# Kernel tuning notes

Hardware: AMD Instinct MI355X
Metric: run time of the kernel (lower is better)

Reference implementation:

```python
import jax, jax.numpy as jnp
import numpy as np

NUM_USER = 20000
NUM_ITEM = 40000
N_NODES = NUM_USER + NUM_ITEM
DIM = 64
V_DIM = 2048
T_DIM = 768
N_EDGES = 1_000_000
K_USER = 40
K_ITEM = 10
N_LAYERS = 2


def setup_inputs() -> dict:
    key = jax.random.key(0)
    ks = iter(jax.random.split(key, 32))

    def xavier(shape):
        s = (2.0 / (shape[0] + shape[-1])) ** 0.5
        return jax.random.normal(next(ks), shape, jnp.float32) * s

    # bipartite user-item interactions, doubled (undirected), as in DRAGON.__init__
    u = jax.random.randint(next(ks), (N_EDGES,), 0, NUM_USER)
    it = jax.random.randint(next(ks), (N_EDGES,), NUM_USER, N_NODES)
    edge_index = jnp.stack([jnp.concatenate([u, it]), jnp.concatenate([it, u])])

    v_feat = jax.random.normal(next(ks), (NUM_ITEM, V_DIM), jnp.float32)
    t_feat = jax.random.normal(next(ks), (NUM_ITEM, T_DIM), jnp.float32)

    # KNN item-item adjacency (top-10 per row) with symmetric-normalized values,
    # mirroring get_knn_adj_mat/compute_normalized_laplacian
    rows = jnp.repeat(jnp.arange(NUM_ITEM), K_ITEM)
    cols = jax.random.randint(next(ks), (NUM_ITEM * K_ITEM,), 0, NUM_ITEM)
    mm_indices = jnp.stack([rows, cols])
    row_sum = jax.ops.segment_sum(jnp.ones(NUM_ITEM * K_ITEM, jnp.float32), rows,
                                  num_segments=NUM_ITEM) + 1e-7
    rinv = row_sum ** -0.5
    mm_values = rinv[rows] * rinv[cols]

    user_graph = jax.random.randint(next(ks), (NUM_USER, K_USER), 0, NUM_USER)
    user_weight_matrix = jax.nn.softmax(
        jax.random.normal(next(ks), (NUM_USER, K_USER), jnp.float32), axis=1)
    weight_u = jax.nn.softmax(
        jax.random.normal(next(ks), (NUM_USER, 2, 1), jnp.float32), axis=1)

    return {
        'edge_index': edge_index,
        'v_feat': v_feat, 't_feat': t_feat,
        'v_pref': xavier((NUM_USER, DIM)), 't_pref': xavier((NUM_USER, DIM)),
        'v_mlp1_w': xavier((V_DIM, 4 * DIM)), 'v_mlp1_b': jnp.zeros(4 * DIM, jnp.float32),
        'v_mlp2_w': xavier((4 * DIM, DIM)), 'v_mlp2_b': jnp.zeros(DIM, jnp.float32),
        't_mlp1_w': xavier((T_DIM, 4 * DIM)), 't_mlp1_b': jnp.zeros(4 * DIM, jnp.float32),
        't_mlp2_w': xavier((4 * DIM, DIM)), 't_mlp2_b': jnp.zeros(DIM, jnp.float32),
        'v_conv_w': xavier((DIM, DIM)), 'v_conv_b': jnp.zeros(DIM, jnp.float32),
        't_conv_w': xavier((DIM, DIM)), 't_conv_b': jnp.zeros(DIM, jnp.float32),
        'weight_u': weight_u,
        'user_graph': user_graph,
        'user_weight_matrix': user_weight_matrix,
        'mm_indices': mm_indices,
        'mm_values': mm_values,
    }


def _l2n(x):
    n = jnp.linalg.norm(x, axis=-1, keepdims=True)
    return x / jnp.maximum(n, 1e-12)


def reference(edge_index, v_feat, t_feat, v_pref, t_pref,
              v_mlp1_w, v_mlp1_b, v_mlp2_w, v_mlp2_b,
              t_mlp1_w, t_mlp1_b, t_mlp2_w, t_mlp2_b,
              v_conv_w, v_conv_b, t_conv_w, t_conv_b,
              weight_u, user_graph, user_weight_matrix,
              mm_indices, mm_values):
    seg = jax.ops.segment_sum
    # GCNConv normalization with self-loops (shared by both branches)
    sl = jnp.arange(N_NODES)
    src = jnp.concatenate([edge_index[0], sl])
    dst = jnp.concatenate([edge_index[1], sl])
    deg = seg(jnp.ones_like(dst, dtype=jnp.float32), dst, num_segments=N_NODES)
    dinv = deg ** -0.5
    norm = (dinv[src] * dinv[dst])[:, None]

    def conv(x, w, b):  # out[dst] += norm * (x @ w)[src], then bias
        return seg(norm * (x @ w)[src], dst, num_segments=N_NODES) + b

    def branch(feat, pref, w1, b1, w2, b2, cw, cb):
        temp = jax.nn.leaky_relu(feat @ w1 + b1) @ w2 + b2  # [I, D]
        x = _l2n(jnp.concatenate([pref, temp], axis=0))      # [N, D]
        h = conv(x, cw, cb)
        h1 = conv(h, cw, cb)
        return x + h + h1

    v_rep = branch(v_feat, v_pref, v_mlp1_w, v_mlp1_b, v_mlp2_w, v_mlp2_b, v_conv_w, v_conv_b)
    t_rep = branch(t_feat, t_pref, t_mlp1_w, t_mlp1_b, t_mlp2_w, t_mlp2_b, t_conv_w, t_conv_b)

    representation = jnp.concatenate([v_rep, t_rep], axis=1)  # [N, 2D]
    wu = weight_u[:, :, 0]  # [U, 2]
    user_rep = jnp.concatenate([wu[:, 0:1] * v_rep[:NUM_USER],
                                wu[:, 1:2] * t_rep[:NUM_USER]], axis=1)  # [U, 2D]
    item_rep = representation[NUM_USER:]  # [I, 2D]

    # User_Graph_sample: weighted sum over sampled user neighborhoods
    h_u = jnp.einsum('uk,ukd->ud', user_weight_matrix, user_rep[user_graph])
    user_rep = user_rep + h_u

    # n_layers of sparse Laplacian propagation over KNN item-item graph
    row, col = mm_indices[0], mm_indices[1]
    h_i = item_rep
    for _ in range(N_LAYERS):
        h_i = seg(mm_values[:, None] * h_i[col], row, num_segments=NUM_ITEM)
    item_rep = item_rep + h_i

    return jnp.concatenate([user_rep, item_rep], axis=0)  # [N, 2D]
```

## Files before the change

### kernel.cpp

```cpp
#include <hip/hip_runtime.h>

#define NUSER 20000
#define NITEM 40000
#define NNODE 60000
#define DIM   64
#define NE    1000000
#define KUSER 40
#define KITEM 10

typedef __attribute__((ext_vector_type(8))) short short8v;
typedef __attribute__((ext_vector_type(4))) float floatx4;

__device__ inline short bf16rne(float f) {
    unsigned u = __builtin_bit_cast(unsigned, f);
    unsigned r = (u + 0x7fffu + ((u >> 16) & 1u)) >> 16;
    return (short)r;
}
__device__ inline unsigned cvt_pk_bf16(float lo, float hi) {
    unsigned r;
    asm("v_cvt_pk_bf16_f32 %0, %1, %2" : "=v"(r) : "v"(lo), "v"(hi));
    return r;
}
__device__ inline float bflo(unsigned v) { return __builtin_bit_cast(float, v << 16); }
__device__ inline float bfhi(unsigned v) { return __builtin_bit_cast(float, v & 0xffff0000u); }

#define CNTB ((NE + 255) / 256)
#define TRB  2944
#define L2NB (NUSER * 2 / 4)
__global__ __launch_bounds__(256) void k_count_transpose_l2n(
        const int* __restrict__ uu, const int* __restrict__ it, int* __restrict__ cnt,
        const float* __restrict__ W1v, const float* __restrict__ W1t,
        const float* __restrict__ W2v, const float* __restrict__ W2t,
        short* __restrict__ Bv, short* __restrict__ Bt,
        short* __restrict__ B2v, short* __restrict__ B2t,
        const float* __restrict__ prefv, const float* __restrict__ preft,
        unsigned* __restrict__ xbf) {
    __shared__ float s[16][17];
    int bid = blockIdx.x;
    if (bid < CNTB) {
        int i = bid * 256 + threadIdx.x;
        if (i >= NE) return;
        atomicAdd(&cnt[uu[i]], 1);
        atomicAdd(&cnt[it[i]], 1);
        return;
    }
    bid -= CNTB;
    if (bid >= TRB) {
        int lb = bid - TRB;
        int lane = threadIdx.x & 63;
        int wg = lb * 4 + (threadIdx.x >> 6);
        int row = wg >> 1, br = wg & 1;
        if (row >= NUSER) return;
        const float* p = br ? preft : prefv;
        float v = p[(size_t)row * 64 + lane];
        float ss = v * v;
        #pragma unroll
        for (int off = 32; off >= 1; off >>= 1) ss += __shfl_xor(ss, off, 64);
        float xn = v / fmaxf(sqrtf(ss), 1e-12f);
        float pn = __shfl_xor(xn, 1, 64);
        if (!(lane & 1))
            xbf[(size_t)row * 64 + (br ? 32 : 0) + (lane >> 1)] = cvt_pk_bf16(xn, pn);
        return;
    }
    const float* B; short* D; int K, N, local;
    if (bid < 2048)      { B = W1v; D = Bv;  K = 2048; N = 256; local = bid; }
    else if (bid < 2816) { B = W1t; D = Bt;  K = 768;  N = 256; local = bid - 2048; }
    else if (bid < 2880) { B = W2v; D = B2v; K = 256;  N = 64;  local = bid - 2816; }
    else                 { B = W2t; D = B2t; K = 256;  N = 64;  local = bid - 2880; }
    int ktiles = K >> 4;
    int k0 = (local % ktiles) * 16, n0 = (local / ktiles) * 16;
    int t = threadIdx.x, tx = t & 15, ty = t >> 4;
    s[ty][tx] = B[(size_t)(k0 + ty) * N + n0 + tx];
    __syncthreads();
    int k = k0 + tx, n = n0 + ty;
    D[(size_t)(k >> 5) * (N * 32) + n * 32 + (k & 31)] = bf16rne(s[tx][ty]);
}

__global__ __launch_bounds__(256) void k_scanA(const int* __restrict__ v, int* __restrict__ excl,
                                               int* __restrict__ bsum, float* __restrict__ dinv, int n) {
    __shared__ int s[256];
    int t = threadIdx.x, i = blockIdx.x * 256 + t;
    int orig = (i < n) ? v[i] : 0;
    if (i < n) dinv[i] = 1.0f / sqrtf((float)(orig + 1));
    s[t] = orig; __syncthreads();
    #pragma unroll
    for (int off = 1; off < 256; off <<= 1) {
        int u = (t >= off) ? s[t - off] : 0;
        __syncthreads();
        s[t] += u;
        __syncthreads();
    }
    if (i < n) excl[i] = s[t] - orig;
    if (t == 255) bsum[blockIdx.x] = s[255];
}

__global__ __launch_bounds__(256) void k_scanB_prep(int* __restrict__ bsum, int nb,
                                                    const float* __restrict__ Wv, const float* __restrict__ Wt,
                                                    const float* __restrict__ bv, const float* __restrict__ bt,
                                                    short* __restrict__ Bcat, float* __restrict__ bw,
                                                    float* __restrict__ bb) {
    __shared__ float Wld[2][64][65];
    __shared__ float W2ld[2][64][65];
    int t = threadIdx.x;
    if (blockIdx.x == 0) {
        int* s = (int*)&Wld[0][0][0];
        int orig = (t < nb) ? bsum[t] : 0;
        s[t] = orig; __syncthreads();
        #pragma unroll
        for (int off = 1; off < 256; off <<= 1) {
            int u = (t >= off) ? s[t - off] : 0;
            __syncthreads();
            s[t] += u;
            __syncthreads();
        }
        if (t < nb) bsum[t] = s[t] - orig;
        return;
    }
    for (int id = t; id < 8192; id += 256) {
        int z = id >> 12, k = (id >> 6) & 63, n = id & 63;
        Wld[z][k][n] = (z ? Wt : Wv)[k * 64 + n];
    }
    __syncthreads();
    for (int id = t; id < 8192; id += 256) {
        int z = id >> 12, k = (id >> 6) & 63, n = id & 63;
        float a = 0.f;
        #pragma unroll 8
        for (int m = 0; m < 64; m++) a += Wld[z][k][m] * Wld[z][m][n];
        W2ld[z][k][n] = a;
    }
    __syncthreads();
    for (int id = t; id < 32768; id += 256) {
        int k = id >> 7, n = id & 127;
        int kb = k >> 6, kk = k & 63;
        float v = 0.f;
        if (kb == 0)      { if (n < 64)  v = Wld[0][kk][n]; }
        else if (kb == 1) { if (n >= 64) v = Wld[1][kk][n - 64]; }
        else if (kb == 2) { if (n < 64)  v = W2ld[0][kk][n]; }
        else              { if (n >= 64) v = W2ld[1][kk][n - 64]; }
        Bcat[(k >> 5) * 4096 + n * 32 + (k & 31)] = bf16rne(v);
    }
    if (t < 128) {
        int z = t >> 6, n = t & 63;
        const float* b = z ? bt : bv;
        float a = 0.f;
        #pragma unroll 8
        for (int k = 0; k < 64; k++) a += b[k] * Wld[z][k][n];
        bw[t] = a;
        bb[t] = 2.f * b[n];
    }
}

__global__ __launch_bounds__(256) void k_scanC(int* __restrict__ excl, const int* __restrict__ bsum,
                                               int* __restrict__ cursor, int n) {
    int i = blockIdx.x * 256 + threadIdx.x;
    if (i < n) {
        int v = excl[i] + bsum[blockIdx.x];
        excl[i] = v;
        cursor[i] = v;
    }
    if (i == 0) excl[n] = 2 * NE;
}

__global__ __launch_bounds__(256) void k_fill_pair(const int* __restrict__ uu, const int* __restrict__ it,
                                                   const float* __restrict__ dinv, int* __restrict__ cursor,
                                                   unsigned* __restrict__ csr_pkd) {
    int i = blockIdx.x * 256 + threadIdx.x;
    if (i >= NE) return;
    int u = uu[i], t = it[i];
    unsigned pku = ((unsigned)(unsigned short)bf16rne(dinv[u]) << 16) | (unsigned)u;
    unsigned pkt = ((unsigned)(unsigned short)bf16rne(dinv[t]) << 16) | (unsigned)t;
    int pos1 = atomicAdd(&cursor[t], 1);
    csr_pkd[pos1] = pku;
    int pos2 = atomicAdd(&cursor[u], 1);
    csr_pkd[pos2] = pkt;
}

#define AP   40
#define MIDP 264
#define MBLK 128
#define VBLKS ((NITEM + MBLK - 1) / MBLK)
__global__ __launch_bounds__(512, 4) void mlp_merged(const float* __restrict__ Av, const float* __restrict__ At,
                                                  const short* __restrict__ B1v, const short* __restrict__ B1t,
                                                  const float* __restrict__ b1v, const float* __restrict__ b1t,
                                                  const short* __restrict__ B2v, const short* __restrict__ B2t,
                                                  const float* __restrict__ b2v, const float* __restrict__ b2t,
                                                  unsigned* __restrict__ xbf) {
    __shared__ short smem[MBLK * MIDP];
    short* As = smem;
    short* Bs = smem + 2 * MBLK * AP;
    const bool isV = blockIdx.x < VBLKS;
    const float* A    = isV ? Av : At;
    const short* B1t_ = isV ? B1v : B1t;
    const float* b1   = isV ? b1v : b1t;
    const short* B2t_ = isV ? B2v : B2t;
    const float* b2   = isV ? b2v : b2t;
    const int K = isV ? 2048 : 768;
    const int boff = isV ? 0 : 32;
    const int rowBase = (isV ? blockIdx.x : blockIdx.x - VBLKS) * MBLK;

    const int tid = threadIdx.x;
    const int lane = tid & 63, wid = tid >> 6;
    const int wr = wid >> 2, wc = wid & 3;

    const int sar = tid >> 2, sac = (tid & 3) * 8;
    int aclamp = rowBase + sar; if (aclamp > NITEM - 1) aclamp = NITEM - 1;
    const float* aptr = A + (size_t)aclamp * K + sac;

    const int fk = (lane >> 4) * 8;
    const int faoff = (wr * 64 + (lane & 15)) * AP + fk;
    const int fboff = (wc * 64 + (lane & 15)) * AP + fk;

    floatx4 acc[4][4];
    #pragma unroll
    for (int m = 0; m < 4; m++)
        #pragma unroll
        for (int n = 0; n < 4; n++) acc[m][n] = (floatx4)0.f;

    float4 ra0, ra1; short8v rb0, rb1;
    float4 na0, na1; short8v nb0, nb1;
    const int nk = K >> 5;

    auto ldgT = [&](int ks, float4& a0, float4& a1, short8v& b0, short8v& b1) {
        const float* ap = aptr + ks * 32;
        a0 = *(const float4*)(ap);
        a1 = *(const float4*)(ap + 4);
        const short* bsrc = B1t_ + (size_t)ks * 8192 + tid * 16;
        b0 = *(const short8v*)(bsrc);
        b1 = *(const short8v*)(bsrc + 8);
    };
    auto stvT = [&](int buf, const float4& a0, const float4& a1, const short8v& b0, const short8v& b1) {
        uint4 av;
        av.x = cvt_pk_bf16(a0.x, a0.y); av.y = cvt_pk_bf16(a0.z, a0.w);
        av.z = cvt_pk_bf16(a1.x, a1.y); av.w = cvt_pk_bf16(a1.z, a1.w);
        *(uint4*)&As[buf * (MBLK * AP) + sar * AP + sac] = av;
        short* bd = &Bs[buf * (256 * AP) + (tid >> 1) * AP + (tid & 1) * 16];
        *(short8v*)(bd) = b0;
        *(short8v*)(bd + 8) = b1;
    };

    ldgT(0, ra0, ra1, rb0, rb1);
    stvT(0, ra0, ra1, rb0, rb1);
    __syncthreads();
    ldgT(1, ra0, ra1, rb0, rb1);
    int cur = 0;
    for (int ks = 0; ks < nk; ++ks) {
        if (ks + 2 < nk) ldgT(ks + 2, na0, na1, nb0, nb1);
        short8v a[4], b[4];
        #pragma unroll
        for (int m = 0; m < 4; m++) a[m] = *(const short8v*)&As[cur * (MBLK * AP) + faoff + m * 16 * AP];
        #pragma unroll
        for (int n = 0; n < 4; n++) b[n] = *(const short8v*)&Bs[cur * (256 * AP) + fboff + n * 16 * AP];
        #pragma unroll
        for (int m = 0; m < 4; m++)
            #pragma unroll
            for (int n = 0; n < 4; n++)
                acc[m][n] = __builtin_amdgcn_mfma_f32_16x16x32_bf16(a[m], b[n], acc[m][n], 0, 0, 0);
        if (ks + 1 < nk) stvT(cur ^ 1, ra0, ra1, rb0, rb1);
        __syncthreads();
        ra0 = na0; ra1 = na1; rb0 = nb0; rb1 = nb1;
        cur ^= 1;
    }

    unsigned* mid32 = (unsigned*)smem;
    float bcol[4];
    #pragma unroll
    for (int n = 0; n < 4; n++) bcol[n] = b1[wc * 64 + n * 16 + (lane & 15)];
    #pragma unroll
    for (int m = 0; m < 4; m++)
        #pragma unroll
        for (int n = 0; n < 4; n++) {
            int col = wc * 64 + n * 16 + (lane & 15);
            #pragma unroll
            for (int q = 0; q < 4; q++) {
                int row = wr * 64 + m * 16 + (lane >> 4) * 4 + q;
                float v = acc[m][n][q] + bcol[n];
                v = v > 0.f ? v : 0.01f * v;
                float pn = __shfl_xor(v, 1, 64);
                if (!(lane & 1)) mid32[row * 132 + (col >> 1)] = cvt_pk_bf16(v, pn);
            }
        }
    __syncthreads();

    const short* mid = smem;
    floatx4 acc2[4];
    #pragma unroll
    for (int n2 = 0; n2 < 4; n2++) acc2[n2] = (floatx4)0.f;
    const int arow = wid * 16 + (lane & 15);
    #pragma unroll
    for (int ks2 = 0; ks2 < 8; ++ks2) {
        short8v af = *(const short8v*)&mid[arow * MIDP + ks2 * 32 + fk];
        const short* bp = B2t_ + ks2 * 2048 + fk;
        short8v bf4[4];
        #pragma unroll
        for (int n2 = 0; n2 < 4; n2++) bf4[n2] = *(const short8v*)(bp + (n2 * 16 + (lane & 15)) * 32);
        #pragma unroll
        for (int n2 = 0; n2 < 4; n2++)
            acc2[n2] = __builtin_amdgcn_mfma_f32_16x16x32_bf16(af, bf4[n2], acc2[n2], 0, 0, 0);
    }

    float b2c[4];
    #pragma unroll
    for (int n2 = 0; n2 < 4; n2++) b2c[n2] = b2[n2 * 16 + (lane & 15)];
    #pragma unroll
    for (int q = 0; q < 4; ++q) {
        float v[4]; float ss = 0.f;
        #pragma unroll
        for (int n2 = 0; n2 < 4; n2++) { v[n2] = acc2[n2][q] + b2c[n2]; ss += v[n2] * v[n2]; }
        ss += __shfl_xor(ss, 1, 64);
        ss += __shfl_xor(ss, 2, 64);
        ss += __shfl_xor(ss, 4, 64);
        ss += __shfl_xor(ss, 8, 64);
        float sc = 1.f / fmaxf(sqrtf(ss), 1e-12f);
        int lr = wid * 16 + (lane >> 4) * 4 + q;
        int grow = NUSER + rowBase + lr;
        bool ok = (rowBase + lr) < NITEM;
        #pragma unroll
        for (int n2 = 0; n2 < 4; n2++) {
            float xn = v[n2] * sc;
            float pn = __shfl_xor(xn, 1, 64);
            if (ok && !(lane & 1))
                xbf[(size_t)grow * 64 + boff + n2 * 8 + ((lane & 15) >> 1)] = cvt_pk_bf16(xn, pn);
        }
    }
}

__global__ __launch_bounds__(256) void k_gather_p(const int* __restrict__ rowptr, const unsigned* __restrict__ csr_pkd,
                                                  const float* __restrict__ dinv, const unsigned* __restrict__ in_bf,
                                                  unsigned* __restrict__ out_bf, float* __restrict__ s_out) {
    int row = blockIdx.x * 4 + (threadIdx.x >> 6);
    int lane = threadIdx.x & 63;
    if (row >= NNODE) return;
    int p0 = rowptr[row], p1 = rowptr[row + 1];
    float dr = dinv[row];
    unsigned sv = in_bf[(size_t)row * 64 + lane];
    float ax0 = dr * bflo(sv), ay0 = dr * bfhi(sv);
    float ax1 = 0.f, ay1 = 0.f;
    float wsum = 0.f;
    for (int p = p0; p < p1; p += 64) {
        int c = p1 - p; if (c > 64) c = 64;
        unsigned pk = (lane < c) ? csr_pkd[p + lane] : 0u;
        wsum += bfhi(pk);
        int j = 0;
        for (; j + 4 <= c; j += 4) {
            unsigned e0 = __shfl(pk, j, 64),     e1 = __shfl(pk, j + 1, 64);
            unsigned e2 = __shfl(pk, j + 2, 64), e3 = __shfl(pk, j + 3, 64);
            unsigned v0 = in_bf[(size_t)(e0 & 0xffffu) * 64 + lane];
            unsigned v1 = in_bf[(size_t)(e1 & 0xffffu) * 64 + lane];
            unsigned v2 = in_bf[(size_t)(e2 & 0xffffu) * 64 + lane];
            unsigned v3 = in_bf[(size_t)(e3 & 0xffffu) * 64 + lane];
            float w0 = bfhi(e0), w1 = bfhi(e1), w2 = bfhi(e2), w3 = bfhi(e3);
            ax0 += w0 * bflo(v0); ay0 += w0 * bfhi(v0);
            ax1 += w1 * bflo(v1); ay1 += w1 * bfhi(v1);
            ax0 += w2 * bflo(v2); ay0 += w2 * bfhi(v2);
            ax1 += w3 * bflo(v3); ay1 += w3 * bfhi(v3);
        }
        for (; j < c; ++j) {
            unsigned e = __shfl(pk, j, 64);
            unsigned v = in_bf[(size_t)(e & 0xffffu) * 64 + lane];
            float w = bfhi(e);
            ax0 += w * bflo(v); ay0 += w * bfhi(v);
        }
    }
    out_bf[(size_t)row * 64 + lane] = cvt_pk_bf16(dr * (ax0 + ax1), dr * (ay0 + ay1));
    #pragma unroll
    for (int o = 32; o >= 1; o >>= 1) wsum += __shfl_xor(wsum, o, 64);
    if (lane == 0) s_out[row] = dr * (dr + wsum);
}

__global__ __launch_bounds__(512) void k_gather2_rep(const int* __restrict__ rowptr, const unsigned* __restrict__ csr_pkd,
                                                     const float* __restrict__ dinv, const unsigned* __restrict__ g1,
                                                     const short* __restrict__ Bcat, const unsigned* __restrict__ x_bf,
                                                     const float* __restrict__ s, const float* __restrict__ bw,
                                                     const float* __restrict__ bb, const float* __restrict__ weight_u,
                                                     float* __restrict__ rep0, unsigned* __restrict__ rep_bf) {
    __shared__ short As[16 * 264];
    const int tid = threadIdx.x, lane = tid & 63, w = tid >> 6;
    const int rowBase = blockIdx.x * 16;

    for (int rr = 0; rr < 2; ++rr) {
        int lrow = w * 2 + rr;
        int row = rowBase + lrow;
        int p0 = rowptr[row], p1 = rowptr[row + 1];
        float dr = dinv[row];
        unsigned sv = g1[(size_t)row * 64 + lane];
        float ax0 = dr * bflo(sv), ay0 = dr * bfhi(sv);
        float ax1 = 0.f, ay1 = 0.f;
        for (int p = p0; p < p1; p += 64) {
            int c = p1 - p; if (c > 64) c = 64;
            unsigned pk = (lane < c) ? csr_pkd[p + lane] : 0u;
            int j = 0;
            for (; j + 4 <= c; j += 4) {
                unsigned e0 = __shfl(pk, j, 64),     e1 = __shfl(pk, j + 1, 64);
                unsigned e2 = __shfl(pk, j + 2, 64), e3 = __shfl(pk, j + 3, 64);
                unsigned v0 = g1[(size_t)(e0 & 0xffffu) * 64 + lane];
                unsigned v1 = g1[(size_t)(e1 & 0xffffu) * 64 + lane];
                unsigned v2 = g1[(size_t)(e2 & 0xffffu) * 64 + lane];
                unsigned v3 = g1[(size_t)(e3 & 0xffffu) * 64 + lane];
                float w0 = bfhi(e0), w1 = bfhi(e1), w2 = bfhi(e2), w3 = bfhi(e3);
                ax0 += w0 * bflo(v0); ay0 += w0 * bfhi(v0);
                ax1 += w1 * bflo(v1); ay1 += w1 * bfhi(v1);
                ax0 += w2 * bflo(v2); ay0 += w2 * bfhi(v2);
                ax1 += w3 * bflo(v3); ay1 += w3 * bfhi(v3);
            }
            for (; j < c; ++j) {
                unsigned e = __shfl(pk, j, 64);
                unsigned v = g1[(size_t)(e & 0xffffu) * 64 + lane];
                float wj = bfhi(e);
                ax0 += wj * bflo(v); ay0 += wj * bfhi(v);
            }
        }
        *(unsigned*)&As[lrow * 264 + 2 * lane] = sv;
        *(unsigned*)&As[lrow * 264 + 128 + 2 * lane] = cvt_pk_bf16(dr * (ax0 + ax1), dr * (ay0 + ay1));
    }
    __syncthreads();

    const int fk = (lane >> 4) * 8;
    floatx4 acc = (floatx4)0.f;
    #pragma unroll
    for (int ks = 0; ks < 8; ++ks) {
        short8v af = *(const short8v*)&As[(lane & 15) * 264 + ks * 32 + fk];
        short8v bf = *(const short8v*)(Bcat + ks * 4096 + (w * 16 + (lane & 15)) * 32 + fk);
        acc = __builtin_amdgcn_mfma_f32_16x16x32_bf16(af, bf, acc, 0, 0, 0);
    }
    const int col = w * 16 + (lane & 15);
    const float bwc = bw[col], bbc = bb[col];
    #pragma unroll
    for (int q = 0; q < 4; ++q) {
        int lrow = (lane >> 4) * 4 + q;
        int row = rowBase + lrow;
        unsigned xw = x_bf[(size_t)row * 64 + (col >> 1)];
        float xval = (col & 1) ? bfhi(xw) : bflo(xw);
        float v = acc[q] + xval + s[row] * bwc + bbc;
        float wu = (row < NUSER) ? weight_u[row * 2 + (col >> 6)] : 1.0f;
        v *= wu;
        rep0[(size_t)row * 128 + col] = v;
        float pn = __shfl_xor(v, 1, 64);
        if (!(lane & 1))
            rep_bf[(size_t)row * 64 + (col >> 1)] = cvt_pk_bf16(v, pn);
    }
}

#define UBLK (NUSER * 64 / 256)
__global__ __launch_bounds__(256) void k_user_item1(const float* __restrict__ rep0, const unsigned* __restrict__ rep_bf,
                                                    const int* __restrict__ ug, const float* __restrict__ uwm,
                                                    const int* __restrict__ mm_col, const float* __restrict__ mm_values,
                                                    float* __restrict__ out, unsigned* __restrict__ tmp_bf) {
    int bid = blockIdx.x;
    if (bid < UBLK) {
        int id = bid * 256 + threadIdx.x;
        int u = id >> 6, lane = id & 63;
        float2 acc = *(const float2*)(rep0 + (size_t)u * 128 + 2 * lane);
        #pragma unroll 4
        for (int k = 0; k < KUSER; k++) {
            int nb = ug[u * KUSER + k];
            float w = uwm[u * KUSER + k];
            unsigned v = rep_bf[(size_t)nb * 64 + lane];
            acc.x += w * bflo(v);
            acc.y += w * bfhi(v);
        }
        *(float2*)(out + (size_t)u * 128 + 2 * lane) = acc;
    } else {
        int id = (bid - UBLK) * 256 + threadIdx.x;
        int r = id >> 6, lane = id & 63;
        float ax = 0.f, ay = 0.f;
        #pragma unroll
        for (int j = 0; j < KITEM; j++) {
            int c = mm_col[r * KITEM + j];
            float w = mm_values[r * KITEM + j];
            unsigned v = rep_bf[(size_t)(NUSER + c) * 64 + lane];
            ax += w * bflo(v);
            ay += w * bfhi(v);
        }
        tmp_bf[(size_t)r * 64 + lane] = cvt_pk_bf16(ax, ay);
    }
}

__global__ __launch_bounds__(256) void k_item2(const float* __restrict__ rep0, const unsigned* __restrict__ tmp_bf,
                                               const int* __restrict__ mm_col, const float* __restrict__ mm_values,
                                               float* __restrict__ out) {
    int id = blockIdx.x * 256 + threadIdx.x;
    int r = id >> 6, lane = id & 63;
    if (r >= NITEM) return;
    float ax = 0.f, ay = 0.f;
    #pragma unroll
    for (int j = 0; j < KITEM; j++) {
        int c = mm_col[r * KITEM + j];
        float w = mm_values[r * KITEM + j];
        unsigned v = tmp_bf[(size_t)c * 64 + lane];
        ax += w * bflo(v);
        ay += w * bfhi(v);
    }
    float2 base = *(const float2*)(rep0 + (size_t)(NUSER + r) * 128 + 2 * lane);
    float2 o;
    o.x = base.x + ax;
    o.y = base.y + ay;
    *(float2*)(out + (size_t)(NUSER + r) * 128 + 2 * lane) = o;
}

extern "C" void kernel_launch(void* const* d_in, const int* in_sizes, int n_in,
                              void* d_out, int out_size, void* d_ws, size_t ws_size,
                              hipStream_t stream) {
    const int*   edge_index = (const int*)d_in[0];
    const float* v_feat   = (const float*)d_in[1];
    const float* t_feat   = (const float*)d_in[2];
    const float* v_pref   = (const float*)d_in[3];
    const float* t_pref   = (const float*)d_in[4];
    const float* v_mlp1_w = (const float*)d_in[5];
    const float* v_mlp1_b = (const float*)d_in[6];
    const float* v_mlp2_w = (const float*)d_in[7];
    const float* v_mlp2_b = (const float*)d_in[8];
    const float* t_mlp1_w = (const float*)d_in[9];
    const float* t_mlp1_b = (const float*)d_in[10];
    const float* t_mlp2_w = (const float*)d_in[11];
    const float* t_mlp2_b = (const float*)d_in[12];
    const float* v_conv_w = (const float*)d_in[13];
    const float* v_conv_b = (const float*)d_in[14];
    const float* t_conv_w = (const float*)d_in[15];
    const float* t_conv_b = (const float*)d_in[16];
    const float* weight_u = (const float*)d_in[17];
    const int*   user_graph = (const int*)d_in[18];
    const float* uwm      = (const float*)d_in[19];
    const int*   mm_indices = (const int*)d_in[20];
    const float* mm_values  = (const float*)d_in[21];
    float* out = (float*)d_out;

    char* wsb = (char*)d_ws;
    size_t off = 0;
    auto alloc = [&](size_t bytes) -> void* {
        void* p = wsb + off;
        off = (off + bytes + 255) & ~(size_t)255;
        return p;
    };
    int*      cnt     = (int*)     alloc(NNODE * 4);
    float*    dinv    = (float*)   alloc(NNODE * 4);
    int*      rowptr  = (int*)     alloc((NNODE + 1) * 4);
    int*      bsum    = (int*)     alloc(256 * 4);
    int*      cursor  = (int*)     alloc(NNODE * 4);
    unsigned* csr_pkd = (unsigned*)alloc((size_t)2 * NE * 4);
    short*    Btw_v   = (short*)   alloc((size_t)2048 * 256 * 2);
    short*    Btw_t   = (short*)   alloc((size_t)768 * 256 * 2);
    short*    W2b_v   = (short*)   alloc((size_t)256 * 64 * 2);
    short*    W2b_t   = (short*)   alloc((size_t)256 * 64 * 2);
    short*    Bcat    = (short*)   alloc((size_t)256 * 128 * 2);
    float*    bw      = (float*)   alloc(128 * 4);
    float*    bb      = (float*)   alloc(128 * 4);
    float*    svec    = (float*)   alloc(NNODE * 4);
    unsigned* x_bf    = (unsigned*)alloc((size_t)NNODE * 64 * 4);
    unsigned* g1      = (unsigned*)alloc((size_t)NNODE * 64 * 4);
    float*    rep0    = (float*)   alloc((size_t)NNODE * 128 * 4);
    unsigned* rep_bf  = (unsigned*)alloc((size_t)NNODE * 64 * 4);
    unsigned* tmp_bf  = (unsigned*)alloc((size_t)NITEM * 64 * 4);
    (void)ws_size; (void)n_in; (void)in_sizes; (void)out_size;

    const int* pairs_u  = edge_index;
    const int* pairs_it = edge_index + NE;
    const int* mm_col = mm_indices + NITEM * KITEM;

    const int NB = (NNODE + 255) / 256;

    hipMemsetAsync(cnt, 0, NNODE * 4, stream);
    k_count_transpose_l2n<<<CNTB + TRB + L2NB, 256, 0, stream>>>(
        pairs_u, pairs_it, cnt, v_mlp1_w, t_mlp1_w, v_mlp2_w, t_mlp2_w,
        Btw_v, Btw_t, W2b_v, W2b_t, v_pref, t_pref, x_bf);
    k_scanA<<<NB, 256, 0, stream>>>(cnt, rowptr, bsum, dinv, NNODE);
    k_scanB_prep<<<2, 256, 0, stream>>>(bsum, NB, v_conv_w, t_conv_w, v_conv_b, t_conv_b, Bcat, bw, bb);
    k_scanC<<<NB, 256, 0, stream>>>(rowptr, bsum, cursor, NNODE);

    k_fill_pair<<<(NE + 255) / 256, 256, 0, stream>>>(pairs_u, pairs_it, dinv, cursor, csr_pkd);
    mlp_merged<<<2 * VBLKS, 512, 0, stream>>>(v_feat, t_feat, Btw_v, Btw_t, v_mlp1_b, t_mlp1_b,
                                              W2b_v, W2b_t, v_mlp2_b, t_mlp2_b, x_bf);

    k_gather_p<<<(NNODE + 3) / 4, 256, 0, stream>>>(rowptr, csr_pkd, dinv, x_bf, g1, svec);
    k_gather2_rep<<<NNODE / 16, 512, 0, stream>>>(rowptr, csr_pkd, dinv, g1, Bcat, x_bf,
                                                  svec, bw, bb, weight_u, rep0, rep_bf);

    k_user_item1<<<UBLK + NITEM * 64 / 256, 256, 0, stream>>>(rep0, rep_bf, user_graph, uwm,
                                                              mm_col, mm_values, out, tmp_bf);
    k_item2<<<NITEM * 64 / 256, 256, 0, stream>>>(rep0, tmp_bf, mm_col, mm_values, out);
}
```

Baseline: 564.2 us.

## Shrink MLP tile to 64 rows and read B fragments directly from global

After: 592.3 us. +5.0%, slower.

```diff
diff --git a/kernel.cpp b/kernel.cpp
--- a/kernel.cpp
+++ b/kernel.cpp
@@ -177,17 +177,15 @@
 
 #define AP   40
 #define MIDP 264
-#define MBLK 128
-#define VBLKS ((NITEM + MBLK - 1) / MBLK)
-__global__ __launch_bounds__(512, 4) void mlp_merged(const float* __restrict__ Av, const float* __restrict__ At,
+#define VBLKS (NITEM / 64)
+__global__ __launch_bounds__(256, 4) void mlp_merged(const float* __restrict__ Av, const float* __restrict__ At,
                                                   const short* __restrict__ B1v, const short* __restrict__ B1t,
                                                   const float* __restrict__ b1v, const float* __restrict__ b1t,
                                                   const short* __restrict__ B2v, const short* __restrict__ B2t,
                                                   const float* __restrict__ b2v, const float* __restrict__ b2t,
                                                   unsigned* __restrict__ xbf) {
-    __shared__ short smem[MBLK * MIDP];
+    __shared__ short smem[64 * MIDP];
     short* As = smem;
-    short* Bs = smem + 2 * MBLK * AP;
     const bool isV = blockIdx.x < VBLKS;
     const float* A    = isV ? Av : At;
     const short* B1t_ = isV ? B1v : B1t;
@@ -196,19 +194,17 @@
     const float* b2   = isV ? b2v : b2t;
     const int K = isV ? 2048 : 768;
     const int boff = isV ? 0 : 32;
-    const int rowBase = (isV ? blockIdx.x : blockIdx.x - VBLKS) * MBLK;
+    const int rowBase = (isV ? blockIdx.x : blockIdx.x - VBLKS) * 64;
 
     const int tid = threadIdx.x;
     const int lane = tid & 63, wid = tid >> 6;
-    const int wr = wid >> 2, wc = wid & 3;
 
     const int sar = tid >> 2, sac = (tid & 3) * 8;
-    int aclamp = rowBase + sar; if (aclamp > NITEM - 1) aclamp = NITEM - 1;
-    const float* aptr = A + (size_t)aclamp * K + sac;
+    const float* aptr = A + (size_t)(rowBase + sar) * K + sac;
 
     const int fk = (lane >> 4) * 8;
-    const int faoff = (wr * 64 + (lane & 15)) * AP + fk;
-    const int fboff = (wc * 64 + (lane & 15)) * AP + fk;
+    const int faoff = (lane & 15) * AP + fk;
+    const int bcol0 = wid * 64 + (lane & 15);
 
     floatx4 acc[4][4];
     #pragma unroll
@@ -216,63 +212,58 @@
         #pragma unroll
         for (int n = 0; n < 4; n++) acc[m][n] = (floatx4)0.f;
 
-    float4 ra0, ra1; short8v rb0, rb1;
-    float4 na0, na1; short8v nb0, nb1;
+    float4 ra0, ra1;
+    float4 na0, na1;
     const int nk = K >> 5;
 
-    auto ldgT = [&](int ks, float4& a0, float4& a1, short8v& b0, short8v& b1) {
+    auto ldgA = [&](int ks, float4& a0, float4& a1) {
         const float* ap = aptr + ks * 32;
         a0 = *(const float4*)(ap);
         a1 = *(const float4*)(ap + 4);
-        const short* bsrc = B1t_ + (size_t)ks * 8192 + tid * 16;
-        b0 = *(const short8v*)(bsrc);
-        b1 = *(const short8v*)(bsrc + 8);
     };
-    auto stvT = [&](int buf, const float4& a0, const float4& a1, const short8v& b0, const short8v& b1) {
+    auto stA = [&](int buf, const float4& a0, const float4& a1) {
         uint4 av;
         av.x = cvt_pk_bf16(a0.x, a0.y); av.y = cvt_pk_bf16(a0.z, a0.w);
         av.z = cvt_pk_bf16(a1.x, a1.y); av.w = cvt_pk_bf16(a1.z, a1.w);
-        *(uint4*)&As[buf * (MBLK * AP) + sar * AP + sac] = av;
-        short* bd = &Bs[buf * (256 * AP) + (tid >> 1) * AP + (tid & 1) * 16];
-        *(short8v*)(bd) = b0;
-        *(short8v*)(bd + 8) = b1;
+        *(uint4*)&As[buf * (64 * AP) + sar * AP + sac] = av;
     };
 
-    ldgT(0, ra0, ra1, rb0, rb1);
-    stvT(0, ra0, ra1, rb0, rb1);
+    ldgA(0, ra0, ra1);
+    stA(0, ra0, ra1);
     __syncthreads();
-    ldgT(1, ra0, ra1, rb0, rb1);
+    ldgA(1, ra0, ra1);
     int cur = 0;
     for (int ks = 0; ks < nk; ++ks) {
-        if (ks + 2 < nk) ldgT(ks + 2, na0, na1, nb0, nb1);
+        if (ks + 2 < nk) ldgA(ks + 2, na0, na1);
         short8v a[4], b[4];
         #pragma unroll
-        for (int m = 0; m < 4; m++) a[m] = *(const short8v*)&As[cur * (MBLK * AP) + faoff + m * 16 * AP];
-        #pragma unroll
-        for (int n = 0; n < 4; n++) b[n] = *(const short8v*)&Bs[cur * (256 * AP) + fboff + n * 16 * AP];
+        for (int n = 0; n < 4; n++)
+            b[n] = *(const short8v*)(B1t_ + (size_t)ks * 8192 + (bcol0 + n * 16) * 32 + fk);
+        #pragma unroll
+        for (int m = 0; m < 4; m++) a[m] = *(const short8v*)&As[cur * (64 * AP) + faoff + m * 16 * AP];
         #pragma unroll
         for (int m = 0; m < 4; m++)
             #pragma unroll
             for (int n = 0; n < 4; n++)
                 acc[m][n] = __builtin_amdgcn_mfma_f32_16x16x32_bf16(a[m], b[n], acc[m][n], 0, 0, 0);
-        if (ks + 1 < nk) stvT(cur ^ 1, ra0, ra1, rb0, rb1);
+        if (ks + 1 < nk) stA(cur ^ 1, ra0, ra1);
         __syncthreads();
-        ra0 = na0; ra1 = na1; rb0 = nb0; rb1 = nb1;
+        ra0 = na0; ra1 = na1;
         cur ^= 1;
     }
 
     unsigned* mid32 = (unsigned*)smem;
     float bcol[4];
     #pragma unroll
-    for (int n = 0; n < 4; n++) bcol[n] = b1[wc * 64 + n * 16 + (lane & 15)];
+    for (int n = 0; n < 4; n++) bcol[n] = b1[wid * 64 + n * 16 + (lane & 15)];
     #pragma unroll
     for (int m = 0; m < 4; m++)
         #pragma unroll
         for (int n = 0; n < 4; n++) {
-            int col = wc * 64 + n * 16 + (lane & 15);
+            int col = wid * 64 + n * 16 + (lane & 15);
             #pragma unroll
             for (int q = 0; q < 4; q++) {
-                int row = wr * 64 + m * 16 + (lane >> 4) * 4 + q;
+                int row = m * 16 + (lane >> 4) * 4 + q;
                 float v = acc[m][n][q] + bcol[n];
                 v = v > 0.f ? v : 0.01f * v;
                 float pn = __shfl_xor(v, 1, 64);
@@ -311,14 +302,12 @@
         ss += __shfl_xor(ss, 4, 64);
         ss += __shfl_xor(ss, 8, 64);
         float sc = 1.f / fmaxf(sqrtf(ss), 1e-12f);
-        int lr = wid * 16 + (lane >> 4) * 4 + q;
-        int grow = NUSER + rowBase + lr;
-        bool ok = (rowBase + lr) < NITEM;
+        int grow = NUSER + rowBase + wid * 16 + (lane >> 4) * 4 + q;
         #pragma unroll
         for (int n2 = 0; n2 < 4; n2++) {
             float xn = v[n2] * sc;
             float pn = __shfl_xor(xn, 1, 64);
-            if (ok && !(lane & 1))
+            if (!(lane & 1))
                 xbf[(size_t)grow * 64 + boff + n2 * 8 + ((lane & 15) >> 1)] = cvt_pk_bf16(xn, pn);
         }
     }
@@ -567,7 +556,7 @@
     k_scanC<<<NB, 256, 0, stream>>>(rowptr, bsum, cursor, NNODE);
 
     k_fill_pair<<<(NE + 255) / 256, 256, 0, stream>>>(pairs_u, pairs_it, dinv, cursor, csr_pkd);
-    mlp_merged<<<2 * VBLKS, 512, 0, stream>>>(v_feat, t_feat, Btw_v, Btw_t, v_mlp1_b, t_mlp1_b,
+    mlp_merged<<<2 * VBLKS, 256, 0, stream>>>(v_feat, t_feat, Btw_v, Btw_t, v_mlp1_b, t_mlp1_b,
                                               W2b_v, W2b_t, v_mlp2_b, t_mlp2_b, x_bf);
 
     k_gather_p<<<(NNODE + 3) / 4, 256, 0, stream>>>(rowptr, csr_pkd, dinv, x_bf, g1, svec);
```

## Load MLP B tiles directly into LDS with XOR-swizzled layout

Applied to the files above, without the earlier changes.

Result: no change. 568.0 us (+0.7%).

```diff
diff --git a/kernel.cpp b/kernel.cpp
--- a/kernel.cpp
+++ b/kernel.cpp
@@ -23,6 +23,11 @@
 }
 __device__ inline float bflo(unsigned v) { return __builtin_bit_cast(float, v << 16); }
 __device__ inline float bfhi(unsigned v) { return __builtin_bit_cast(float, v & 0xffff0000u); }
+
+__device__ inline void gload_lds16(const void* g, void* lds) {
+    __builtin_amdgcn_global_load_lds((const __attribute__((address_space(1))) void*)g,
+                                     (__attribute__((address_space(3))) void*)lds, 16, 0, 0);
+}
 
 #define CNTB ((NE + 255) / 256)
 #define TRB  2944
@@ -73,7 +78,9 @@
     s[ty][tx] = B[(size_t)(k0 + ty) * N + n0 + tx];
     __syncthreads();
     int k = k0 + tx, n = n0 + ty;
-    D[(size_t)(k >> 5) * (N * 32) + n * 32 + (k & 31)] = bf16rne(s[tx][ty]);
+    int idx = n * 32 + (k & 31);
+    if (N == 256) idx ^= ((idx >> 5) & 7) << 3;
+    D[(size_t)(k >> 5) * (N * 32) + idx] = bf16rne(s[tx][ty]);
 }
 
 __global__ __launch_bounds__(256) void k_scanA(const int* __restrict__ v, int* __restrict__ excl,
@@ -187,7 +194,7 @@
                                                   unsigned* __restrict__ xbf) {
     __shared__ short smem[MBLK * MIDP];
     short* As = smem;
-    short* Bs = smem + 2 * MBLK * AP;
+    short* BsLin = smem + 2 * MBLK * AP;
     const bool isV = blockIdx.x < VBLKS;
     const float* A    = isV ? Av : At;
     const short* B1t_ = isV ? B1v : B1t;
@@ -208,7 +215,12 @@
 
     const int fk = (lane >> 4) * 8;
     const int faoff = (wr * 64 + (lane & 15)) * AP + fk;
-    const int fboff = (wc * 64 + (lane & 15)) * AP + fk;
+    int fbo[4];
+    #pragma unroll
+    for (int n = 0; n < 4; n++) {
+        int bsh = (wc * 64 + (lane & 15) + n * 16) * 32 + fk;
+        fbo[n] = bsh ^ (((bsh >> 5) & 7) << 3);
+    }
 
     floatx4 acc[4][4];
     #pragma unroll
@@ -216,48 +228,45 @@
         #pragma unroll
         for (int n = 0; n < 4; n++) acc[m][n] = (floatx4)0.f;
 
-    float4 ra0, ra1; short8v rb0, rb1;
-    float4 na0, na1; short8v nb0, nb1;
+    float4 ra0, ra1;
     const int nk = K >> 5;
 
-    auto ldgT = [&](int ks, float4& a0, float4& a1, short8v& b0, short8v& b1) {
+    auto ldB = [&](int ks, int buf) {
+        short* ldsbase = BsLin + buf * 8192 + wid * 1024;
+        const short* gsrc = B1t_ + (size_t)ks * 8192 + wid * 1024 + lane * 8;
+        gload_lds16(gsrc, ldsbase);
+        gload_lds16(gsrc + 512, ldsbase + 512);
+    };
+    auto ldgA = [&](int ks) {
         const float* ap = aptr + ks * 32;
-        a0 = *(const float4*)(ap);
-        a1 = *(const float4*)(ap + 4);
-        const short* bsrc = B1t_ + (size_t)ks * 8192 + tid * 16;
-        b0 = *(const short8v*)(bsrc);
-        b1 = *(const short8v*)(bsrc + 8);
+        ra0 = *(const float4*)(ap);
+        ra1 = *(const float4*)(ap + 4);
     };
-    auto stvT = [&](int buf, const float4& a0, const float4& a1, const short8v& b0, const short8v& b1) {
+    auto stA = [&](int buf) {
         uint4 av;
-        av.x = cvt_pk_bf16(a0.x, a0.y); av.y = cvt_pk_bf16(a0.z, a0.w);
-        av.z = cvt_pk_bf16(a1.x, a1.y); av.w = cvt_pk_bf16(a1.z, a1.w);
+        av.x = cvt_pk_bf16(ra0.x, ra0.y); av.y = cvt_pk_bf16(ra0.z, ra0.w);
+        av.z = cvt_pk_bf16(ra1.x, ra1.y); av.w = cvt_pk_bf16(ra1.z, ra1.w);
         *(uint4*)&As[buf * (MBLK * AP) + sar * AP + sac] = av;
-        short* bd = &Bs[buf * (256 * AP) + (tid >> 1) * AP + (tid & 1) * 16];
-        *(short8v*)(bd) = b0;
-        *(short8v*)(bd + 8) = b1;
     };
 
-    ldgT(0, ra0, ra1, rb0, rb1);
-    stvT(0, ra0, ra1, rb0, rb1);
+    ldB(0, 0);
+    ldgA(0); stA(0);
     __syncthreads();
-    ldgT(1, ra0, ra1, rb0, rb1);
     int cur = 0;
     for (int ks = 0; ks < nk; ++ks) {
-        if (ks + 2 < nk) ldgT(ks + 2, na0, na1, nb0, nb1);
+        if (ks + 1 < nk) { ldB(ks + 1, cur ^ 1); ldgA(ks + 1); }
         short8v a[4], b[4];
         #pragma unroll
         for (int m = 0; m < 4; m++) a[m] = *(const short8v*)&As[cur * (MBLK * AP) + faoff + m * 16 * AP];
         #pragma unroll
-        for (int n = 0; n < 4; n++) b[n] = *(const short8v*)&Bs[cur * (256 * AP) + fboff + n * 16 * AP];
+        for (int n = 0; n < 4; n++) b[n] = *(const short8v*)&BsLin[cur * 8192 + fbo[n]];
         #pragma unroll
         for (int m = 0; m < 4; m++)
             #pragma unroll
             for (int n = 0; n < 4; n++)
                 acc[m][n] = __builtin_amdgcn_mfma_f32_16x16x32_bf16(a[m], b[n], acc[m][n], 0, 0, 0);
-        if (ks + 1 < nk) stvT(cur ^ 1, ra0, ra1, rb0, rb1);
+        if (ks + 1 < nk) stA(cur ^ 1);
         __syncthreads();
-        ra0 = na0; ra1 = na1; rb0 = nb0; rb1 = nb1;
         cur ^= 1;
     }
 
```
